# Optimization experiments

Hardware: AMD Instinct MI355X
Metric: run time of the kernel (lower is better)

Reference implementation:

```python
import jax, jax.numpy as jnp
import numpy as np

EPS = 1e-5
J = 17


def build_adj(num_joints=J):
    edges = [(0, 1), (1, 2), (1, 3), (3, 4), (4, 5), (1, 6), (6, 7), (7, 8),
             (0, 9), (9, 10), (10, 11), (0, 12), (12, 13), (13, 14)]
    if num_joints > 15:
        edges.extend([(11, 15), (14, 16)])
    adj = np.eye(num_joints, dtype=np.float32)
    for i, j in edges:
        if i < num_joints and j < num_joints:
            adj[i, j] = 1.0
            adj[j, i] = 1.0
    adj = adj / adj.sum(axis=1, keepdims=True)
    return jnp.asarray(adj)


def _bn(x, g, b, m, v):
    # inference-mode BatchNorm2d over channel axis 1 of (B,C,T,J)
    scale = (g / jnp.sqrt(v + EPS))[None, :, None, None]
    shift = (b - m * g / jnp.sqrt(v + EPS))[None, :, None, None]
    return x * scale + shift


def _conv1x1(x, w, b):
    # x: (B,C,T,J), w: (O,C) -> (B,O,T,J)
    return jnp.einsum('oc,bctj->botj', w, x) + b[None, :, None, None]


def _tconv(x, w, b):
    # temporal conv kernel (3,1), padding (1,0); x: (B,C,T,J), w: (O,C,3)
    y = jax.lax.conv_general_dilated(
        x, w[:, :, :, None], window_strides=(1, 1),
        padding=[(1, 1), (0, 0)],
        dimension_numbers=('NCHW', 'OIHW', 'NCHW'))
    return y + b[None, :, None, None]


def _block(x, adj, sw, sb, sg, sbb, sm, sv, tw, tb, tg, tbb, tm, tv,
           rw, rb, rg, rbb, rm, rv):
    residual = _bn(_conv1x1(x, rw, rb), rg, rbb, rm, rv)
    y = jnp.einsum('bctj,jk->bctk', x, adj)
    y = jax.nn.relu(_bn(_conv1x1(y, sw, sb), sg, sbb, sm, sv))
    y = _bn(_tconv(y, tw, tb), tg, tbb, tm, tv)
    return jax.nn.relu(y + residual)  # dropout is identity in eval mode


def setup_inputs() -> dict:
    key = jax.random.key(0)
    ks = iter(jax.random.split(key, 64))
    B, T = 16, 2048

    def randn(shape, s=0.1):
        return jax.random.normal(next(ks), shape, dtype=jnp.float32) * s

    def bn_params(c):
        g = 1.0 + randn((c,), 0.05)
        b = randn((c,), 0.05)
        m = randn((c,), 0.1)
        v = jax.random.uniform(next(ks), (c,), minval=0.5, maxval=1.5)
        return g, b, m, v

    inp = {
        'x': jax.random.normal(next(ks), (B, 3, T, J), dtype=jnp.float32),
        'adj': build_adj(J),
    }
    # block 0: 3 -> 64
    inp['b0_sw'] = randn((64, 3)); inp['b0_sb'] = randn((64,), 0.02)
    inp['b0_sg'], inp['b0_sbb'], inp['b0_sm'], inp['b0_sv'] = bn_params(64)
    inp['b0_tw'] = randn((64, 64, 3), 0.05); inp['b0_tb'] = randn((64,), 0.02)
    inp['b0_tg'], inp['b0_tbb'], inp['b0_tm'], inp['b0_tv'] = bn_params(64)
    inp['b0_rw'] = randn((64, 3)); inp['b0_rb'] = randn((64,), 0.02)
    inp['b0_rg'], inp['b0_rbb'], inp['b0_rm'], inp['b0_rv'] = bn_params(64)
    # block 1: 64 -> 128
    inp['b1_sw'] = randn((128, 64), 0.05); inp['b1_sb'] = randn((128,), 0.02)
    inp['b1_sg'], inp['b1_sbb'], inp['b1_sm'], inp['b1_sv'] = bn_params(128)
    inp['b1_tw'] = randn((128, 128, 3), 0.03); inp['b1_tb'] = randn((128,), 0.02)
    inp['b1_tg'], inp['b1_tbb'], inp['b1_tm'], inp['b1_tv'] = bn_params(128)
    inp['b1_rw'] = randn((128, 64), 0.05); inp['b1_rb'] = randn((128,), 0.02)
    inp['b1_rg'], inp['b1_rbb'], inp['b1_rm'], inp['b1_rv'] = bn_params(128)
    # projection 128 -> 128
    inp['proj_w'] = randn((128, 128), 0.05); inp['proj_b'] = randn((128,), 0.02)
    return inp


def reference(x, adj,
              b0_sw, b0_sb, b0_sg, b0_sbb, b0_sm, b0_sv,
              b0_tw, b0_tb, b0_tg, b0_tbb, b0_tm, b0_tv,
              b0_rw, b0_rb, b0_rg, b0_rbb, b0_rm, b0_rv,
              b1_sw, b1_sb, b1_sg, b1_sbb, b1_sm, b1_sv,
              b1_tw, b1_tb, b1_tg, b1_tbb, b1_tm, b1_tv,
              b1_rw, b1_rb, b1_rg, b1_rbb, b1_rm, b1_rv,
              proj_w, proj_b):
    y = _block(x, adj, b0_sw, b0_sb, b0_sg, b0_sbb, b0_sm, b0_sv,
               b0_tw, b0_tb, b0_tg, b0_tbb, b0_tm, b0_tv,
               b0_rw, b0_rb, b0_rg, b0_rbb, b0_rm, b0_rv)
    y = _block(y, adj, b1_sw, b1_sb, b1_sg, b1_sbb, b1_sm, b1_sv,
               b1_tw, b1_tb, b1_tg, b1_tbb, b1_tm, b1_tv,
               b1_rw, b1_rb, b1_rg, b1_rbb, b1_rm, b1_rv)
    y = y.mean(axis=-1)            # (B, C, T)
    y = y.transpose(0, 2, 1)       # (B, T, C)
    return jnp.einsum('btc,ec->bte', y, proj_w) + proj_b  # (B, T, embed)
```

## Files before the change

### kernel.cpp

```cpp
#include <hip/hip_runtime.h>
#include <hip/hip_bf16.h>
#include <stdint.h>

typedef __attribute__((ext_vector_type(8))) short bf16x8;
typedef __attribute__((ext_vector_type(4))) float f32x4;

#define EPSB 1e-5f

#define W0TE_B   0u
#define W1SB_B   24576u
#define W1E_B    40960u
#define W1R_B    139264u
#define PROJW_B  155648u
#define WS0F_B   188416u
#define WR0F_B   189440u
#define BS0F_B   190464u
#define CB0F_B   190720u
#define BS1F_B   190976u
#define CB1F_B   191488u
#define SPT_B    192000u
#define MEANS_B  193536u
#define Y0_PERB  4456448ull

__device__ __forceinline__ float bf2f(unsigned int u16v) {
    union { unsigned int i; float f; } v; v.i = u16v << 16; return v.f;
}
__device__ __forceinline__ unsigned short f2bf(float f) {
    unsigned int x = __float_as_uint(f);
    x = x + 0x7fffu + ((x >> 16) & 1u);
    return (unsigned short)(x >> 16);
}
__device__ __forceinline__ unsigned pk2(float a, float b) {
    union { __hip_bfloat162 h; unsigned u; } v;
    v.h = __float22bfloat162_rn(make_float2(a, b));
    return v.u;
}
__device__ __forceinline__ int div17(int p) { return (p * 241) >> 12; }

struct PrepArgs {
    const float *sw0,*sb0,*sg0,*sbb0,*sm0,*sv0;
    const float *tw0,*tb0,*tg0,*tbb0,*tm0,*tv0;
    const float *rw0,*rb0,*rg0,*rbb0,*rm0,*rv0;
    const float *sw1,*sb1,*sg1,*sbb1,*sm1,*sv1;
    const float *tw1,*tb1,*tg1,*tbb1,*tm1,*tv1;
    const float *rw1,*rb1,*rg1,*rbb1,*rm1,*rv1;
    const float *projw;
    const float *adj;
    unsigned char* ws;
};

__global__ void prep_kernel(PrepArgs a) {
    const int g = blockIdx.x * 256 + threadIdx.x;
    unsigned short* W0TE  = (unsigned short*)(a.ws + W0TE_B);
    unsigned short* W1SBp = (unsigned short*)(a.ws + W1SB_B);
    unsigned short* W1Ep  = (unsigned short*)(a.ws + W1E_B);
    unsigned short* W1Rp  = (unsigned short*)(a.ws + W1R_B);
    unsigned short* PROJW = (unsigned short*)(a.ws + PROJW_B);
    float* WS0F = (float*)(a.ws + WS0F_B);
    float* WR0F = (float*)(a.ws + WR0F_B);
    float* BS0F = (float*)(a.ws + BS0F_B);
    float* CB0F = (float*)(a.ws + CB0F_B);
    float* BS1F = (float*)(a.ws + BS1F_B);
    float* CB1F = (float*)(a.ws + CB1F_B);
    float2* SPT = (float2*)(a.ws + SPT_B);

    if (g < 64) {
        int o = g;
        float scs = a.sg0[o] / sqrtf(a.sv0[o] + EPSB);
        BS0F[o] = scs * (a.sb0[o] - a.sm0[o]) + a.sbb0[o];
        for (int c = 0; c < 4; c++) WS0F[o*4+c] = (c < 3) ? scs * a.sw0[o*3+c] : 0.f;
        float tct = a.tg0[o] / sqrtf(a.tv0[o] + EPSB);
        float rcr = a.rg0[o] / sqrtf(a.rv0[o] + EPSB);
        CB0F[o] = tct * (a.tb0[o] - a.tm0[o]) + a.tbb0[o]
                + rcr * (a.rb0[o] - a.rm0[o]) + a.rbb0[o];
        for (int c = 0; c < 4; c++) WR0F[o*4+c] = (c < 3) ? rcr * a.rw0[o*3+c] : 0.f;
    } else if (g < 192) {
        int o = g - 64;
        float scs = a.sg1[o] / sqrtf(a.sv1[o] + EPSB);
        BS1F[o] = scs * (a.sb1[o] - a.sm1[o]) + a.sbb1[o];
        float tct = a.tg1[o] / sqrtf(a.tv1[o] + EPSB);
        float rcr = a.rg1[o] / sqrtf(a.rv1[o] + EPSB);
        CB1F[o] = tct * (a.tb1[o] - a.tm1[o]) + a.tbb1[o]
                + rcr * (a.rb1[o] - a.rm1[o]) + a.rbb1[o];
    } else if (g < 12480) {
        int idx = g - 192;
        int o = idx / 192, k = idx % 192, tap = k >> 6, c = k & 63;
        float tct = a.tg0[o] / sqrtf(a.tv0[o] + EPSB);
        W0TE[o*192 + k] = f2bf(tct * a.tw0[(o*64 + c)*3 + tap]);
    } else if (g < 20672) {
        int idx = g - 12480;
        int o = idx >> 6, c = idx & 63;
        float scs = a.sg1[o] / sqrtf(a.sv1[o] + EPSB);
        W1SBp[o*64 + c] = f2bf(scs * a.sw1[o*64 + c]);
    } else if (g < 69824) {
        int idx = g - 20672;
        int h = idx / 24576, r = idx % 24576;
        int o = r / 192, k = r % 192, tap = k >> 6, c = (h << 6) + (k & 63);
        float tct = a.tg1[o] / sqrtf(a.tv1[o] + EPSB);
        W1Ep[(h*128 + o)*192 + k] = f2bf(tct * a.tw1[(o*128 + c)*3 + tap]);
    } else if (g < 78016) {
        int idx = g - 69824;
        int o = idx >> 6, c = idx & 63;
        float rcr = a.rg1[o] / sqrtf(a.rv1[o] + EPSB);
        W1Rp[o*64 + c] = f2bf(rcr * a.rw1[o*64 + c]);
    } else if (g < 94400) {
        int idx = g - 78016;
        PROJW[idx] = f2bf(a.projw[idx]);
    } else if (g < 94417) {
        int j = g - 94400;
        int cnt = 0;
        for (int k = 0; k < 17; k++) {
            float v = a.adj[k*17 + j];
            if (v != 0.0f && cnt < 8) {
                SPT[j*8 + cnt] = make_float2(v, __uint_as_float((unsigned)k));
                cnt++;
            }
        }
        for (; cnt < 8; cnt++) SPT[j*8 + cnt] = make_float2(0.f, __uint_as_float(0u));
    }
}

__launch_bounds__(256, 3)
__global__ void b0_kernel(const float* __restrict__ x,
                          const unsigned char* __restrict__ ws,
                          unsigned short* __restrict__ Y0, int b0base) {
    __shared__ float xt[510];
    __shared__ float xg[510];
    __shared__ float2 spt[136];
    __shared__ float Ws0s[256], Wr0s[256], bs0s[64], cb0s[64];
    __shared__ __align__(16) unsigned short s0[170*72];
    __shared__ __align__(16) unsigned short yst[136*72];

    const int tid = threadIdx.x;
    const int b_loc = blockIdx.x >> 8;
    const int b = b0base + b_loc;
    const int t0 = (blockIdx.x & 255) << 3;
    const int Pb = (t0 - 1) * 17;

    const int w = tid >> 6, l = tid & 63, lr = l & 15, lg = l >> 4;
    const int n = w*16 + lr;

    const unsigned short* W0TE = (const unsigned short*)(ws + W0TE_B);
    bf16x8 bfr[6];
    #pragma unroll
    for (int ks = 0; ks < 6; ks++)
        bfr[ks] = *(const bf16x8*)&W0TE[n*192 + ks*32 + lg*8];

    if (tid < 136) {
        float2 raw = ((const float2*)(ws + SPT_B))[tid];
        spt[tid] = make_float2(raw.x, __uint_as_float(__float_as_uint(raw.y) * 4u));
    }
    Ws0s[tid] = ((const float*)(ws + WS0F_B))[tid];
    Wr0s[tid] = ((const float*)(ws + WR0F_B))[tid];
    if (tid < 64) {
        bs0s[tid] = ((const float*)(ws + BS0F_B))[tid];
        cb0s[tid] = ((const float*)(ws + CB0F_B))[tid];
    }
    #pragma unroll
    for (int it = 0; it < 2; it++) {
        int idx = tid + it*256;
        if (idx < 510) {
            int c = idx / 170, r = idx - c*170;
            int P = Pb + r;
            float v = 0.f;
            if (P >= 0 && P < 34816) v = x[(size_t)(b*3 + c)*34816 + P];
            xt[idx] = v;
        }
    }
    __syncthreads();
    #pragma unroll
    for (int it = 0; it < 2; it++) {
        int idx = tid + it*256;
        if (idx < 510) {
            int c = idx / 170, r = idx - c*170;
            int j = r - 17*div17(r);
            const char* rowb = (const char*)&xt[c*170 + (r - j)];
            float acc = 0.f;
            #pragma unroll
            for (int i = 0; i < 8; i++) {
                float2 e = spt[j*8 + i];
                acc += e.x * *(const float*)(rowb + __float_as_uint(e.y));
            }
            xg[idx] = acc;
        }
    }
    __syncthreads();
    #pragma unroll
    for (int it = 0; it < 11; it++) {
        int idx = tid + it*256;
        if (idx < 2720) {
            int r = idx >> 4, cg = idx & 15, o0 = cg*4;
            int P = Pb + r;
            uint2 pkv = make_uint2(0u, 0u);
            if (P >= 0 && P < 34816) {
                float a0 = xg[r], a1 = xg[170 + r], a2 = xg[340 + r];
                float v0 = fmaxf(bs0s[o0]   + Ws0s[(o0  )*4]*a0 + Ws0s[(o0  )*4+1]*a1 + Ws0s[(o0  )*4+2]*a2, 0.f);
                float v1 = fmaxf(bs0s[o0+1] + Ws0s[(o0+1)*4]*a0 + Ws0s[(o0+1)*4+1]*a1 + Ws0s[(o0+1)*4+2]*a2, 0.f);
                float v2 = fmaxf(bs0s[o0+2] + Ws0s[(o0+2)*4]*a0 + Ws0s[(o0+2)*4+1]*a1 + Ws0s[(o0+2)*4+2]*a2, 0.f);
                float v3 = fmaxf(bs0s[o0+3] + Ws0s[(o0+3)*4]*a0 + Ws0s[(o0+3)*4+1]*a1 + Ws0s[(o0+3)*4+2]*a2, 0.f);
                pkv.x = pk2(v0, v1); pkv.y = pk2(v2, v3);
            }
            *(uint2*)&s0[r*72 + o0] = pkv;
        }
    }
    __syncthreads();
    {
        const float wr0 = Wr0s[n*4], wr1 = Wr0s[n*4+1], wr2 = Wr0s[n*4+2];
        const float cbn = cb0s[n];
        for (int mb = 0; mb < 9; mb++) {
            const int ra = mb*16 + lr;
            f32x4 acc = {0.f, 0.f, 0.f, 0.f};
            #pragma unroll
            for (int ks = 0; ks < 6; ks++) {
                int row = ra + (ks >> 1)*17; if (row > 169) row = 169;
                const int c0 = ((ks & 1) << 5) + lg*8;
                acc = __builtin_amdgcn_mfma_f32_16x16x32_bf16(
                    *(const bf16x8*)&s0[row*72 + c0], bfr[ks], acc, 0, 0, 0);
            }
            const int mbase = mb*16 + lg*4;
            #pragma unroll
            for (int i = 0; i < 4; i++) {
                const int m = mbase + i;
                if (m < 136) {
                    float v = acc[i] + cbn + wr0*xt[m+17] + wr1*xt[170+m+17] + wr2*xt[340+m+17];
                    yst[m*72 + n] = f2bf(fmaxf(v, 0.f));
                }
            }
        }
    }
    __syncthreads();
    #pragma unroll
    for (int it = 0; it < 5; it++) {
        int idx = tid + it*256;
        if (idx < 1088) {
            int m = idx >> 3, seg = idx & 7;
            uint4 v = *(const uint4*)&yst[m*72 + seg*8];
            *(uint4*)&Y0[((size_t)b_loc*34816 + t0*17 + m)*64 + seg*8] = v;
        }
    }
}

__launch_bounds__(512, 2)
__global__ void b1_kernel(const unsigned char* __restrict__ ws,
                          const unsigned short* __restrict__ Y0,
                          unsigned short* __restrict__ MEANS) {
    __shared__ __align__(16) unsigned short buf[24480];
    __shared__ float2 spt[136];
    __shared__ float cb1s[128], bs1s[128];

    unsigned short* bufA = buf;
    unsigned short* ygs  = buf + 12240;
    unsigned short* y1   = buf;

    const int tid = threadIdx.x;
    const int b_loc = blockIdx.x >> 5;
    const int ck = blockIdx.x & 31;

    const unsigned short* W1SBp = (const unsigned short*)(ws + W1SB_B);
    const unsigned short* W1Ep  = (const unsigned short*)(ws + W1E_B);
    const unsigned short* W1Rp  = (const unsigned short*)(ws + W1R_B);

    const int w = tid >> 6, l = tid & 63, lr = l & 15, lg = l >> 4;
    const int n = w*16 + lr;
    const int sNt = w & 3, sMh = w >> 2;
    const int nloc_s = sNt*16 + lr;

    if (tid < 136) {
        float2 raw = ((const float2*)(ws + SPT_B))[tid];
        spt[tid] = make_float2(raw.x, __uint_as_float(__float_as_uint(raw.y) * 144u));
    }
    if (tid < 128) {
        cb1s[tid] = ((const float*)(ws + CB1F_B))[tid];
        bs1s[tid] = ((const float*)(ws + BS1F_B))[tid];
    }
    bf16x8 rb0 = *(const bf16x8*)&W1Rp[n*64 + lg*8];
    bf16x8 rb1 = *(const bf16x8*)&W1Rp[n*64 + 32 + lg*8];

    uint4 pf[3];
    {
        const int t0n = ck << 6;
        #pragma unroll
        for (int s = 0; s < 3; s++) {
            int idx = tid + s*512;
            uint4 v = make_uint4(0u,0u,0u,0u);
            if (idx < 1360) {
                int p = idx >> 3, seg = idx & 7;
                int P = (t0n - 1)*17 + p;
                if (P >= 0 && P < 34816)
                    v = *(const uint4*)&Y0[((size_t)b_loc*34816 + P)*64 + seg*8];
            }
            pf[s] = v;
        }
    }

    for (int tt = 0; tt < 8; tt++) {
        const int t0 = (ck << 6) + (tt << 3);
        const int Pb = (t0 - 1) * 17;

        #pragma unroll
        for (int s = 0; s < 3; s++) {
            int idx = tid + s*512;
            if (idx < 1360) {
                int p = idx >> 3, seg = idx & 7;
                *(uint4*)&bufA[p*72 + seg*8] = pf[s];
            }
        }
        __syncthreads();

        if (tt < 7) {
            const int t0n = t0 + 8;
            #pragma unroll
            for (int s = 0; s < 3; s++) {
                int idx = tid + s*512;
                uint4 v = make_uint4(0u,0u,0u,0u);
                if (idx < 1360) {
                    int p = idx >> 3, seg = idx & 7;
                    int P = (t0n - 1)*17 + p;
                    if (P >= 0 && P < 34816)
                        v = *(const uint4*)&Y0[((size_t)b_loc*34816 + P)*64 + seg*8];
                }
                pf[s] = v;
            }
        }
        bf16x8 bfh[6];
        #pragma unroll
        for (int ks = 0; ks < 6; ks++)
            bfh[ks] = *(const bf16x8*)&W1Ep[n*192 + ks*32 + lg*8];

        f32x4 tacc[9];
        #pragma unroll
        for (int mb = 0; mb < 9; mb++) {
            const int row = mb*16 + lr + 17;
            f32x4 acc = {0.f, 0.f, 0.f, 0.f};
            acc = __builtin_amdgcn_mfma_f32_16x16x32_bf16(*(const bf16x8*)&bufA[row*72 + lg*8],      rb0, acc, 0, 0, 0);
            acc = __builtin_amdgcn_mfma_f32_16x16x32_bf16(*(const bf16x8*)&bufA[row*72 + 32 + lg*8], rb1, acc, 0, 0, 0);
            tacc[mb] = acc;
        }
        #pragma unroll
        for (int q = 0; q < 6; q++) {
            int idx = tid + q*512;
            if (idx < 2720) {
                int p = idx >> 4, cg = idx & 15;
                int j = p - 17*div17(p);
                const char* rowb = (const char*)bufA + (p - j)*144 + cg*8;
                float a0=0.f, a1=0.f, a2=0.f, a3=0.f;
                #pragma unroll
                for (int i = 0; i < 8; i++) {
                    float2 e = spt[j*8 + i];
                    uint2 u = *(const uint2*)(rowb + __float_as_uint(e.y));
                    a0 += e.x * __uint_as_float(u.x << 16);
                    a1 += e.x * __uint_as_float(u.x & 0xffff0000u);
                    a2 += e.x * __uint_as_float(u.y << 16);
                    a3 += e.x * __uint_as_float(u.y & 0xffff0000u);
                }
                uint2 o; o.x = pk2(a0, a1); o.y = pk2(a2, a3);
                *(uint2*)&ygs[p*72 + cg*4] = o;
            }
        }
        __syncthreads();

        {
            bf16x8 sbA = *(const bf16x8*)&W1SBp[(nloc_s)*64 + lg*8];
            bf16x8 sbB = *(const bf16x8*)&W1SBp[(nloc_s)*64 + 32 + lg*8];
            const int mbE = sMh ? 11 : 6;
            for (int mb = sMh ? 6 : 0; mb < mbE; mb++) {
                int ra = mb*16 + lr; if (ra > 169) ra = 169;
                f32x4 sa = {0.f, 0.f, 0.f, 0.f};
                sa = __builtin_amdgcn_mfma_f32_16x16x32_bf16(*(const bf16x8*)&ygs[ra*72 + lg*8],      sbA, sa, 0, 0, 0);
                sa = __builtin_amdgcn_mfma_f32_16x16x32_bf16(*(const bf16x8*)&ygs[ra*72 + 32 + lg*8], sbB, sa, 0, 0, 0);
                const int mbase = mb*16 + lg*4;
                #pragma unroll
                for (int i = 0; i < 4; i++) {
                    int m = mbase + i;
                    if (m < 170) {
                        int P = Pb + m;
                        float v = (P >= 0 && P < 34816) ? fmaxf(sa[i] + bs1s[nloc_s], 0.f) : 0.f;
                        bufA[m*72 + nloc_s] = f2bf(v);
                    }
                }
            }
        }
        __syncthreads();

        #pragma unroll
        for (int mb = 0; mb < 9; mb++) {
            const int ma = mb*16 + lr;
            f32x4 acc = tacc[mb];
            #pragma unroll
            for (int ks = 0; ks < 6; ks++) {
                int row = ma + (ks >> 1)*17; if (row > 169) row = 169;
                const int c0 = ((ks & 1) << 5) + lg*8;
                acc = __builtin_amdgcn_mfma_f32_16x16x32_bf16(
                    *(const bf16x8*)&bufA[row*72 + c0], bfh[ks], acc, 0, 0, 0);
            }
            tacc[mb] = acc;
        }
        __syncthreads();

        #pragma unroll
        for (int ks = 0; ks < 6; ks++)
            bfh[ks] = *(const bf16x8*)&W1Ep[(128 + n)*192 + ks*32 + lg*8];
        {
            bf16x8 sbA = *(const bf16x8*)&W1SBp[(64 + nloc_s)*64 + lg*8];
            bf16x8 sbB = *(const bf16x8*)&W1SBp[(64 + nloc_s)*64 + 32 + lg*8];
            const int mbE = sMh ? 11 : 6;
            for (int mb = sMh ? 6 : 0; mb < mbE; mb++) {
                int ra = mb*16 + lr; if (ra > 169) ra = 169;
                f32x4 sa = {0.f, 0.f, 0.f, 0.f};
                sa = __builtin_amdgcn_mfma_f32_16x16x32_bf16(*(const bf16x8*)&ygs[ra*72 + lg*8],      sbA, sa, 0, 0, 0);
                sa = __builtin_amdgcn_mfma_f32_16x16x32_bf16(*(const bf16x8*)&ygs[ra*72 + 32 + lg*8], sbB, sa, 0, 0, 0);
                const int mbase = mb*16 + lg*4;
                #pragma unroll
                for (int i = 0; i < 4; i++) {
                    int m = mbase + i;
                    if (m < 170) {
                        int P = Pb + m;
                        float v = (P >= 0 && P < 34816) ? fmaxf(sa[i] + bs1s[64 + nloc_s], 0.f) : 0.f;
                        bufA[m*72 + nloc_s] = f2bf(v);
                    }
                }
            }
        }
        __syncthreads();

        #pragma unroll
        for (int mb = 0; mb < 9; mb++) {
            const int ma = mb*16 + lr;
            f32x4 acc = tacc[mb];
            #pragma unroll
            for (int ks = 0; ks < 6; ks++) {
                int row = ma + (ks >> 1)*17; if (row > 169) row = 169;
                const int c0 = ((ks & 1) << 5) + lg*8;
                acc = __builtin_amdgcn_mfma_f32_16x16x32_bf16(
                    *(const bf16x8*)&bufA[row*72 + c0], bfh[ks], acc, 0, 0, 0);
            }
            tacc[mb] = acc;
        }
        __syncthreads();

        #pragma unroll
        for (int mb = 0; mb < 9; mb++) {
            const int mbase = mb*16 + lg*4;
            #pragma unroll
            for (int i = 0; i < 4; i++) {
                int m = mbase + i;
                if (m < 136)
                    y1[m*132 + n] = f2bf(fmaxf(tacc[mb][i] + cb1s[n], 0.f));
            }
        }
        __syncthreads();

        {
            const int t = tid >> 6, n2 = (tid & 63) * 2;
            float s0v = 0.f, s1v = 0.f;
            #pragma unroll
            for (int jj = 0; jj < 17; jj++) {
                unsigned u = *(const unsigned*)&y1[(t*17 + jj)*132 + n2];
                s0v += __uint_as_float(u << 16);
                s1v += __uint_as_float(u & 0xffff0000u);
            }
            const float sc = 1.f / 17.f;
            *(unsigned*)&MEANS[((size_t)(b_loc*2048 + t0 + t))*128 + n2] = pk2(s0v*sc, s1v*sc);
        }
        __syncthreads();
    }
}

__launch_bounds__(256, 3)
__global__ void proj_kernel(const unsigned short* __restrict__ MEANS,
                            const unsigned char* __restrict__ ws,
                            const float* __restrict__ projb,
                            float* __restrict__ outp, int bt_base) {
    __shared__ __align__(16) unsigned short As[128*136];
    __shared__ float pbs[128];

    const int tid = threadIdx.x;
    const int m0 = blockIdx.x * 128;
    const int w = tid >> 6, l = tid & 63, lr = l & 15, lg = l >> 4;
    const unsigned short* PROJW = (const unsigned short*)(ws + PROJW_B);

    if (tid < 128) pbs[tid] = projb[tid];
    #pragma unroll
    for (int it = 0; it < 8; it++) {
        int idx = tid + it*256;
        int m = idx >> 4, seg = idx & 15;
        *(uint4*)&As[m*136 + seg*8] = *(const uint4*)&MEANS[(size_t)(m0 + m)*128 + seg*8];
    }
    __syncthreads();

    f32x4 acc[8][2];
    #pragma unroll
    for (int et = 0; et < 8; et++) {
        const int e = et*16 + lr;
        bf16x8 bf[4];
        #pragma unroll
        for (int kf = 0; kf < 4; kf++)
            bf[kf] = *(const bf16x8*)&PROJW[e*128 + kf*32 + lg*8];
        #pragma unroll
        for (int m2 = 0; m2 < 2; m2++) {
            const int ra = (w*2 + m2)*16 + lr;
            f32x4 a = {0.f, 0.f, 0.f, 0.f};
            #pragma unroll
            for (int kf = 0; kf < 4; kf++)
                a = __builtin_amdgcn_mfma_f32_16x16x32_bf16(
                    *(const bf16x8*)&As[ra*136 + kf*32 + lg*8], bf[kf], a, 0, 0, 0);
            acc[et][m2] = a;
        }
    }
    #pragma unroll
    for (int et = 0; et < 8; et++) {
        const int e = et*16 + lr;
        const float pb = pbs[e];
        #pragma unroll
        for (int m2 = 0; m2 < 2; m2++) {
            const int mbase = (w*2 + m2)*16 + lg*4;
            #pragma unroll
            for (int i = 0; i < 4; i++) {
                const int m = mbase + i;
                outp[(size_t)(bt_base + m0 + m)*128 + e] = acc[et][m2][i] + pb;
            }
        }
    }
}

extern "C" void kernel_launch(void* const* d_in, const int* in_sizes, int n_in,
                              void* d_out, int out_size, void* d_ws, size_t ws_size,
                              hipStream_t stream) {
    const float* x     = (const float*)d_in[0];
    const float* adj   = (const float*)d_in[1];
    const float* projb = (const float*)d_in[39];
    unsigned char* ws  = (unsigned char*)d_ws;

    PrepArgs pa;
    pa.sw0 = (const float*)d_in[2];  pa.sb0  = (const float*)d_in[3];
    pa.sg0 = (const float*)d_in[4];  pa.sbb0 = (const float*)d_in[5];
    pa.sm0 = (const float*)d_in[6];  pa.sv0  = (const float*)d_in[7];
    pa.tw0 = (const float*)d_in[8];  pa.tb0  = (const float*)d_in[9];
    pa.tg0 = (const float*)d_in[10]; pa.tbb0 = (const float*)d_in[11];
    pa.tm0 = (const float*)d_in[12]; pa.tv0  = (const float*)d_in[13];
    pa.rw0 = (const float*)d_in[14]; pa.rb0  = (const float*)d_in[15];
    pa.rg0 = (const float*)d_in[16]; pa.rbb0 = (const float*)d_in[17];
    pa.rm0 = (const float*)d_in[18]; pa.rv0  = (const float*)d_in[19];
    pa.sw1 = (const float*)d_in[20]; pa.sb1  = (const float*)d_in[21];
    pa.sg1 = (const float*)d_in[22]; pa.sbb1 = (const float*)d_in[23];
    pa.sm1 = (const float*)d_in[24]; pa.sv1  = (const float*)d_in[25];
    pa.tw1 = (const float*)d_in[26]; pa.tb1  = (const float*)d_in[27];
    pa.tg1 = (const float*)d_in[28]; pa.tbb1 = (const float*)d_in[29];
    pa.tm1 = (const float*)d_in[30]; pa.tv1  = (const float*)d_in[31];
    pa.rw1 = (const float*)d_in[32]; pa.rb1  = (const float*)d_in[33];
    pa.rg1 = (const float*)d_in[34]; pa.rbb1 = (const float*)d_in[35];
    pa.rm1 = (const float*)d_in[36]; pa.rv1  = (const float*)d_in[37];
    pa.projw = (const float*)d_in[38];
    pa.adj = adj;
    pa.ws = ws;

    prep_kernel<<<dim3(369), dim3(256), 0, stream>>>(pa);

    int chunk = 16;
    while (chunk > 1 &&
           (size_t)MEANS_B + (size_t)chunk * (524288ull + Y0_PERB) > ws_size)
        chunk >>= 1;

    unsigned short* MEANSp = (unsigned short*)(ws + MEANS_B);
    unsigned short* Y0p    = (unsigned short*)(ws + MEANS_B + (size_t)chunk * 524288ull);

    for (int cb = 0; cb < 16; cb += chunk) {
        b0_kernel<<<dim3(chunk * 256), dim3(256), 0, stream>>>(x, ws, Y0p, cb);
        b1_kernel<<<dim3(chunk * 32), dim3(512), 0, stream>>>(ws, Y0p, MEANSp);
        proj_kernel<<<dim3(chunk * 16), dim3(256), 0, stream>>>(MEANSp, ws, projb, (float*)d_out, cb * 2048);
    }
}
```

Before: 395.4 us.

## Move block-1 graph aggregation into b0 kernel and fuse mean into MFMA epilogue

The block-0 kernel now also computes the adjacency aggregation of its output and writes it as a second bf16 tensor YG. Block-1 loads YG and Y0 directly instead of recomputing the aggregation in shared memory. Block-1 also keeps separate buffers so several barriers disappear, doubles its grid with half the time steps per block, and computes the joint mean with register shuffles instead of staging y1 through LDS. The cost is an extra global write and read of an activation-sized tensor, plus larger workspace and LDS use per block.

Measured after the change: 370.5 us. -6.3%, faster.

```diff
diff --git a/kernel.cpp b/kernel.cpp
--- a/kernel.cpp
+++ b/kernel.cpp
@@ -20,6 +20,7 @@
 #define CB1F_B   191488u
 #define SPT_B    192000u
 #define MEANS_B  193536u
+#define MEANS_PERB 524288ull
 #define Y0_PERB  4456448ull
 
 __device__ __forceinline__ float bf2f(unsigned int u16v) {
@@ -123,10 +124,12 @@
 __launch_bounds__(256, 3)
 __global__ void b0_kernel(const float* __restrict__ x,
                           const unsigned char* __restrict__ ws,
-                          unsigned short* __restrict__ Y0, int b0base) {
+                          unsigned short* __restrict__ Y0,
+                          unsigned short* __restrict__ YG, int b0base) {
     __shared__ float xt[510];
     __shared__ float xg[510];
-    __shared__ float2 spt[136];
+    __shared__ float2 sptA[136];
+    __shared__ float2 sptB[136];
     __shared__ float Ws0s[256], Wr0s[256], bs0s[64], cb0s[64];
     __shared__ __align__(16) unsigned short s0[170*72];
     __shared__ __align__(16) unsigned short yst[136*72];
@@ -148,7 +151,8 @@
 
     if (tid < 136) {
         float2 raw = ((const float2*)(ws + SPT_B))[tid];
-        spt[tid] = make_float2(raw.x, __uint_as_float(__float_as_uint(raw.y) * 4u));
+        sptA[tid] = make_float2(raw.x, __uint_as_float(__float_as_uint(raw.y) * 4u));
+        sptB[tid] = make_float2(raw.x, __uint_as_float(__float_as_uint(raw.y) * 144u));
     }
     Ws0s[tid] = ((const float*)(ws + WS0F_B))[tid];
     Wr0s[tid] = ((const float*)(ws + WR0F_B))[tid];
@@ -178,7 +182,7 @@
             float acc = 0.f;
             #pragma unroll
             for (int i = 0; i < 8; i++) {
-                float2 e = spt[j*8 + i];
+                float2 e = sptA[j*8 + i];
                 acc += e.x * *(const float*)(rowb + __float_as_uint(e.y));
             }
             xg[idx] = acc;
@@ -238,23 +242,43 @@
             *(uint4*)&Y0[((size_t)b_loc*34816 + t0*17 + m)*64 + seg*8] = v;
         }
     }
+    #pragma unroll
+    for (int it = 0; it < 9; it++) {
+        int idx = tid + it*256;
+        if (idx < 2176) {
+            int p = idx >> 4, cg = idx & 15;
+            int j = p - 17*div17(p);
+            const char* rowb = (const char*)yst + (p - j)*144 + cg*8;
+            float a0=0.f, a1=0.f, a2=0.f, a3=0.f;
+            #pragma unroll
+            for (int i = 0; i < 8; i++) {
+                float2 e = sptB[j*8 + i];
+                uint2 u = *(const uint2*)(rowb + __float_as_uint(e.y));
+                a0 += e.x * __uint_as_float(u.x << 16);
+                a1 += e.x * __uint_as_float(u.x & 0xffff0000u);
+                a2 += e.x * __uint_as_float(u.y << 16);
+                a3 += e.x * __uint_as_float(u.y & 0xffff0000u);
+            }
+            uint2 o; o.x = pk2(a0, a1); o.y = pk2(a2, a3);
+            *(uint2*)&YG[((size_t)b_loc*34816 + t0*17 + p)*64 + cg*4] = o;
+        }
+    }
 }
 
 __launch_bounds__(512, 2)
 __global__ void b1_kernel(const unsigned char* __restrict__ ws,
                           const unsigned short* __restrict__ Y0,
+                          const unsigned short* __restrict__ YG,
                           unsigned short* __restrict__ MEANS) {
-    __shared__ __align__(16) unsigned short buf[24480];
-    __shared__ float2 spt[136];
+    __shared__ __align__(16) unsigned short smem[36720];
+    unsigned short* ybuf  = smem;
+    unsigned short* ygbuf = smem + 12240;
+    unsigned short* s0buf = smem + 24480;
     __shared__ float cb1s[128], bs1s[128];
 
-    unsigned short* bufA = buf;
-    unsigned short* ygs  = buf + 12240;
-    unsigned short* y1   = buf;
-
     const int tid = threadIdx.x;
-    const int b_loc = blockIdx.x >> 5;
-    const int ck = blockIdx.x & 31;
+    const int b_loc = blockIdx.x >> 6;
+    const int ck = blockIdx.x & 63;
 
     const unsigned short* W1SBp = (const unsigned short*)(ws + W1SB_B);
     const unsigned short* W1Ep  = (const unsigned short*)(ws + W1E_B);
@@ -265,10 +289,6 @@
     const int sNt = w & 3, sMh = w >> 2;
     const int nloc_s = sNt*16 + lr;
 
-    if (tid < 136) {
-        float2 raw = ((const float2*)(ws + SPT_B))[tid];
-        spt[tid] = make_float2(raw.x, __uint_as_float(__float_as_uint(raw.y) * 144u));
-    }
     if (tid < 128) {
         cb1s[tid] = ((const float*)(ws + CB1F_B))[tid];
         bs1s[tid] = ((const float*)(ws + BS1F_B))[tid];
@@ -276,191 +296,164 @@
     bf16x8 rb0 = *(const bf16x8*)&W1Rp[n*64 + lg*8];
     bf16x8 rb1 = *(const bf16x8*)&W1Rp[n*64 + 32 + lg*8];
 
-    uint4 pf[3];
-    {
-        const int t0n = ck << 6;
+    uint4 pf[5];
+    auto PF = [&](int t0n) {
+        const int Pb = t0n*17 - 17;
         #pragma unroll
-        for (int s = 0; s < 3; s++) {
+        for (int s = 0; s < 5; s++) {
             int idx = tid + s*512;
             uint4 v = make_uint4(0u,0u,0u,0u);
             if (idx < 1360) {
                 int p = idx >> 3, seg = idx & 7;
-                int P = (t0n - 1)*17 + p;
+                int P = Pb + p;
                 if (P >= 0 && P < 34816)
-                    v = *(const uint4*)&Y0[((size_t)b_loc*34816 + P)*64 + seg*8];
+                    v = *(const uint4*)&YG[((size_t)b_loc*34816 + P)*64 + seg*8];
+            } else if (idx < 2448) {
+                int p = (idx - 1360) >> 3, seg = (idx - 1360) & 7;
+                v = *(const uint4*)&Y0[((size_t)b_loc*34816 + t0n*17 + p)*64 + seg*8];
             }
             pf[s] = v;
         }
-    }
-
-    for (int tt = 0; tt < 8; tt++) {
-        const int t0 = (ck << 6) + (tt << 3);
+    };
+    PF(ck << 5);
+
+    for (int tt = 0; tt < 4; tt++) {
+        const int t0 = (ck << 5) + (tt << 3);
         const int Pb = (t0 - 1) * 17;
 
         #pragma unroll
-        for (int s = 0; s < 3; s++) {
+        for (int s = 0; s < 5; s++) {
             int idx = tid + s*512;
             if (idx < 1360) {
                 int p = idx >> 3, seg = idx & 7;
-                *(uint4*)&bufA[p*72 + seg*8] = pf[s];
+                *(uint4*)&ygbuf[p*72 + seg*8] = pf[s];
+            } else if (idx < 2448) {
+                int p = (idx - 1360) >> 3, seg = (idx - 1360) & 7;
+                *(uint4*)&ybuf[(17 + p)*72 + seg*8] = pf[s];
             }
         }
         __syncthreads();
 
-        if (tt < 7) {
-            const int t0n = t0 + 8;
-            #pragma unroll
-            for (int s = 0; s < 3; s++) {
-                int idx = tid + s*512;
-                uint4 v = make_uint4(0u,0u,0u,0u);
-                if (idx < 1360) {
-                    int p = idx >> 3, seg = idx & 7;
-                    int P = (t0n - 1)*17 + p;
-                    if (P >= 0 && P < 34816)
-                        v = *(const uint4*)&Y0[((size_t)b_loc*34816 + P)*64 + seg*8];
-                }
-                pf[s] = v;
-            }
-        }
-        bf16x8 bfh[6];
-        #pragma unroll
-        for (int ks = 0; ks < 6; ks++)
-            bfh[ks] = *(const bf16x8*)&W1Ep[n*192 + ks*32 + lg*8];
+        if (tt < 3) PF(t0 + 8);
 
         f32x4 tacc[9];
         #pragma unroll
         for (int mb = 0; mb < 9; mb++) {
-            const int row = mb*16 + lr + 17;
+            const int row = 17 + mb*16 + lr;
             f32x4 acc = {0.f, 0.f, 0.f, 0.f};
-            acc = __builtin_amdgcn_mfma_f32_16x16x32_bf16(*(const bf16x8*)&bufA[row*72 + lg*8],      rb0, acc, 0, 0, 0);
-            acc = __builtin_amdgcn_mfma_f32_16x16x32_bf16(*(const bf16x8*)&bufA[row*72 + 32 + lg*8], rb1, acc, 0, 0, 0);
+            acc = __builtin_amdgcn_mfma_f32_16x16x32_bf16(*(const bf16x8*)&ybuf[row*72 + lg*8],      rb0, acc, 0, 0, 0);
+            acc = __builtin_amdgcn_mfma_f32_16x16x32_bf16(*(const bf16x8*)&ybuf[row*72 + 32 + lg*8], rb1, acc, 0, 0, 0);
             tacc[mb] = acc;
         }
-        #pragma unroll
-        for (int q = 0; q < 6; q++) {
-            int idx = tid + q*512;
-            if (idx < 2720) {
-                int p = idx >> 4, cg = idx & 15;
-                int j = p - 17*div17(p);
-                const char* rowb = (const char*)bufA + (p - j)*144 + cg*8;
-                float a0=0.f, a1=0.f, a2=0.f, a3=0.f;
-                #pragma unroll
-                for (int i = 0; i < 8; i++) {
-                    float2 e = spt[j*8 + i];
-                    uint2 u = *(const uint2*)(rowb + __float_as_uint(e.y));
-                    a0 += e.x * __uint_as_float(u.x << 16);
-                    a1 += e.x * __uint_as_float(u.x & 0xffff0000u);
-                    a2 += e.x * __uint_as_float(u.y << 16);
-                    a3 += e.x * __uint_as_float(u.y & 0xffff0000u);
-                }
-                uint2 o; o.x = pk2(a0, a1); o.y = pk2(a2, a3);
-                *(uint2*)&ygs[p*72 + cg*4] = o;
-            }
-        }
-        __syncthreads();
-
         {
             bf16x8 sbA = *(const bf16x8*)&W1SBp[(nloc_s)*64 + lg*8];
             bf16x8 sbB = *(const bf16x8*)&W1SBp[(nloc_s)*64 + 32 + lg*8];
+            const float bias = bs1s[nloc_s];
             const int mbE = sMh ? 11 : 6;
             for (int mb = sMh ? 6 : 0; mb < mbE; mb++) {
                 int ra = mb*16 + lr; if (ra > 169) ra = 169;
                 f32x4 sa = {0.f, 0.f, 0.f, 0.f};
-                sa = __builtin_amdgcn_mfma_f32_16x16x32_bf16(*(const bf16x8*)&ygs[ra*72 + lg*8],      sbA, sa, 0, 0, 0);
-                sa = __builtin_amdgcn_mfma_f32_16x16x32_bf16(*(const bf16x8*)&ygs[ra*72 + 32 + lg*8], sbB, sa, 0, 0, 0);
+                sa = __builtin_amdgcn_mfma_f32_16x16x32_bf16(*(const bf16x8*)&ygbuf[ra*72 + lg*8],      sbA, sa, 0, 0, 0);
+                sa = __builtin_amdgcn_mfma_f32_16x16x32_bf16(*(const bf16x8*)&ygbuf[ra*72 + 32 + lg*8], sbB, sa, 0, 0, 0);
                 const int mbase = mb*16 + lg*4;
                 #pragma unroll
                 for (int i = 0; i < 4; i++) {
                     int m = mbase + i;
                     if (m < 170) {
                         int P = Pb + m;
-                        float v = (P >= 0 && P < 34816) ? fmaxf(sa[i] + bs1s[nloc_s], 0.f) : 0.f;
-                        bufA[m*72 + nloc_s] = f2bf(v);
+                        float v = (P >= 0 && P < 34816) ? fmaxf(sa[i] + bias, 0.f) : 0.f;
+                        s0buf[m*72 + nloc_s] = f2bf(v);
                     }
                 }
             }
         }
         __syncthreads();
 
-        #pragma unroll
-        for (int mb = 0; mb < 9; mb++) {
-            const int ma = mb*16 + lr;
-            f32x4 acc = tacc[mb];
-            #pragma unroll
-            for (int ks = 0; ks < 6; ks++) {
-                int row = ma + (ks >> 1)*17; if (row > 169) row = 169;
-                const int c0 = ((ks & 1) << 5) + lg*8;
-                acc = __builtin_amdgcn_mfma_f32_16x16x32_bf16(
-                    *(const bf16x8*)&bufA[row*72 + c0], bfh[ks], acc, 0, 0, 0);
-            }
-            tacc[mb] = acc;
-        }
-        __syncthreads();
-
-        #pragma unroll
-        for (int ks = 0; ks < 6; ks++)
-            bfh[ks] = *(const bf16x8*)&W1Ep[(128 + n)*192 + ks*32 + lg*8];
+        {
+            bf16x8 bfh[6];
+            #pragma unroll
+            for (int ks = 0; ks < 6; ks++)
+                bfh[ks] = *(const bf16x8*)&W1Ep[n*192 + ks*32 + lg*8];
+            #pragma unroll
+            for (int mb = 0; mb < 9; mb++) {
+                const int ma = mb*16 + lr;
+                f32x4 acc = tacc[mb];
+                #pragma unroll
+                for (int ks = 0; ks < 6; ks++) {
+                    int row = ma + (ks >> 1)*17; if (row > 169) row = 169;
+                    const int c0 = ((ks & 1) << 5) + lg*8;
+                    acc = __builtin_amdgcn_mfma_f32_16x16x32_bf16(
+                        *(const bf16x8*)&s0buf[row*72 + c0], bfh[ks], acc, 0, 0, 0);
+                }
+                tacc[mb] = acc;
+            }
+        }
         {
             bf16x8 sbA = *(const bf16x8*)&W1SBp[(64 + nloc_s)*64 + lg*8];
             bf16x8 sbB = *(const bf16x8*)&W1SBp[(64 + nloc_s)*64 + 32 + lg*8];
+            const float bias = bs1s[64 + nloc_s];
             const int mbE = sMh ? 11 : 6;
             for (int mb = sMh ? 6 : 0; mb < mbE; mb++) {
                 int ra = mb*16 + lr; if (ra > 169) ra = 169;
                 f32x4 sa = {0.f, 0.f, 0.f, 0.f};
-                sa = __builtin_amdgcn_mfma_f32_16x16x32_bf16(*(const bf16x8*)&ygs[ra*72 + lg*8],      sbA, sa, 0, 0, 0);
-                sa = __builtin_amdgcn_mfma_f32_16x16x32_bf16(*(const bf16x8*)&ygs[ra*72 + 32 + lg*8], sbB, sa, 0, 0, 0);
+                sa = __builtin_amdgcn_mfma_f32_16x16x32_bf16(*(const bf16x8*)&ygbuf[ra*72 + lg*8],      sbA, sa, 0, 0, 0);
+                sa = __builtin_amdgcn_mfma_f32_16x16x32_bf16(*(const bf16x8*)&ygbuf[ra*72 + 32 + lg*8], sbB, sa, 0, 0, 0);
                 const int mbase = mb*16 + lg*4;
                 #pragma unroll
                 for (int i = 0; i < 4; i++) {
                     int m = mbase + i;
                     if (m < 170) {
                         int P = Pb + m;
-                        float v = (P >= 0 && P < 34816) ? fmaxf(sa[i] + bs1s[64 + nloc_s], 0.f) : 0.f;
-                        bufA[m*72 + nloc_s] = f2bf(v);
+                        float v = (P >= 0 && P < 34816) ? fmaxf(sa[i] + bias, 0.f) : 0.f;
+                        ybuf[m*72 + nloc_s] = f2bf(v);
                     }
                 }
             }
         }
         __syncthreads();
 
-        #pragma unroll
-        for (int mb = 0; mb < 9; mb++) {
-            const int ma = mb*16 + lr;
-            f32x4 acc = tacc[mb];
-            #pragma unroll
-            for (int ks = 0; ks < 6; ks++) {
-                int row = ma + (ks >> 1)*17; if (row > 169) row = 169;
-                const int c0 = ((ks & 1) << 5) + lg*8;
-                acc = __builtin_amdgcn_mfma_f32_16x16x32_bf16(
-                    *(const bf16x8*)&bufA[row*72 + c0], bfh[ks], acc, 0, 0, 0);
-            }
-            tacc[mb] = acc;
-        }
-        __syncthreads();
-
-        #pragma unroll
-        for (int mb = 0; mb < 9; mb++) {
-            const int mbase = mb*16 + lg*4;
-            #pragma unroll
-            for (int i = 0; i < 4; i++) {
-                int m = mbase + i;
-                if (m < 136)
-                    y1[m*132 + n] = f2bf(fmaxf(tacc[mb][i] + cb1s[n], 0.f));
-            }
-        }
-        __syncthreads();
-
         {
-            const int t = tid >> 6, n2 = (tid & 63) * 2;
-            float s0v = 0.f, s1v = 0.f;
-            #pragma unroll
-            for (int jj = 0; jj < 17; jj++) {
-                unsigned u = *(const unsigned*)&y1[(t*17 + jj)*132 + n2];
-                s0v += __uint_as_float(u << 16);
-                s1v += __uint_as_float(u & 0xffff0000u);
-            }
-            const float sc = 1.f / 17.f;
-            *(unsigned*)&MEANS[((size_t)(b_loc*2048 + t0 + t))*128 + n2] = pk2(s0v*sc, s1v*sc);
+            bf16x8 bfh[6];
+            #pragma unroll
+            for (int ks = 0; ks < 6; ks++)
+                bfh[ks] = *(const bf16x8*)&W1Ep[(128 + n)*192 + ks*32 + lg*8];
+            #pragma unroll
+            for (int mb = 0; mb < 9; mb++) {
+                const int ma = mb*16 + lr;
+                f32x4 acc = tacc[mb];
+                #pragma unroll
+                for (int ks = 0; ks < 6; ks++) {
+                    int row = ma + (ks >> 1)*17; if (row > 169) row = 169;
+                    const int c0 = ((ks & 1) << 5) + lg*8;
+                    acc = __builtin_amdgcn_mfma_f32_16x16x32_bf16(
+                        *(const bf16x8*)&ybuf[row*72 + c0], bfh[ks], acc, 0, 0, 0);
+                }
+                tacc[mb] = acc;
+            }
+        }
+        {
+            const float cb = cb1s[n];
+            #pragma unroll
+            for (int t = 0; t < 8; t++) {
+                float s = 0.f;
+                #pragma unroll
+                for (int mb = 0; mb < 9; mb++) {
+                    #pragma unroll
+                    for (int i = 0; i < 4; i++) {
+                        const int mlo = mb*16 + i;
+                        if (mlo + 12 >= t*17 && mlo <= t*17 + 16 && mlo < 136) {
+                            int m = mlo + lg*4;
+                            bool in = (m >= t*17) && (m <= t*17 + 16) && (m < 136);
+                            float v = fmaxf(tacc[mb][i] + cb, 0.f);
+                            s += in ? v : 0.f;
+                        }
+                    }
+                }
+                s += __shfl_xor(s, 16, 64);
+                s += __shfl_xor(s, 32, 64);
+                if ((t & 3) == lg)
+                    MEANS[((size_t)(b_loc*2048 + t0 + t))*128 + n] = f2bf(s * (1.f/17.f));
+            }
         }
         __syncthreads();
     }
@@ -556,17 +549,17 @@
 
     prep_kernel<<<dim3(369), dim3(256), 0, stream>>>(pa);
 
+    const size_t perb = MEANS_PERB + 2ull * Y0_PERB;
     int chunk = 16;
-    while (chunk > 1 &&
-           (size_t)MEANS_B + (size_t)chunk * (524288ull + Y0_PERB) > ws_size)
-        chunk >>= 1;
+    while (chunk > 1 && (size_t)MEANS_B + (size_t)chunk * perb > ws_size) chunk >>= 1;
 
     unsigned short* MEANSp = (unsigned short*)(ws + MEANS_B);
-    unsigned short* Y0p    = (unsigned short*)(ws + MEANS_B + (size_t)chunk * 524288ull);
+    unsigned short* Y0p    = (unsigned short*)(ws + MEANS_B + (size_t)chunk * MEANS_PERB);
+    unsigned short* YGp    = (unsigned short*)((unsigned char*)Y0p + (size_t)chunk * Y0_PERB);
 
     for (int cb = 0; cb < 16; cb += chunk) {
-        b0_kernel<<<dim3(chunk * 256), dim3(256), 0, stream>>>(x, ws, Y0p, cb);
-        b1_kernel<<<dim3(chunk * 32), dim3(512), 0, stream>>>(ws, Y0p, MEANSp);
+        b0_kernel<<<dim3(chunk * 256), dim3(256), 0, stream>>>(x, ws, Y0p, YGp, cb);
+        b1_kernel<<<dim3(chunk * 64), dim3(512), 0, stream>>>(ws, Y0p, YGp, MEANSp);
         proj_kernel<<<dim3(chunk * 16), dim3(256), 0, stream>>>(MEANSp, ws, projb, (float*)d_out, cb * 2048);
     }
 }
```
